# Performance work log

Measured on AMD Instinct MI355X. Metric: run time of the kernel, lower is better.

Reference implementation:

```python
import jax, jax.numpy as jnp
import numpy as np

B0, H0, W0 = 2, 64, 64
C0, E0, N0, R0 = 96, 192, 16, 6


def sass(H, W):
    L = H * W
    o1, o2, o3, o4 = [], [], [], []
    o1i = [-1] * L; o2i = [-1] * L; o3i = [-1] * L; o4i = [-1] * L
    if H % 2 == 1:
        i, j = H - 1, W - 1; jd = 'left'
    else:
        i, j = H - 1, 0; jd = 'right'
    while i > -1:
        idx = i * W + j
        o1i[idx] = len(o1); o1.append(idx)
        if jd == 'right':
            if j < W - 1: j += 1
            else: i -= 1; jd = 'left'
        elif j > 0: j -= 1
        else: i -= 1; jd = 'right'
    i, j = 0, 0; idd = 'down'
    while j < W:
        idx = i * W + j
        o2i[idx] = len(o2); o2.append(idx)
        if idd == 'down':
            if i < H - 1: i += 1
            else: j += 1; idd = 'up'
        elif i > 0: i -= 1
        else: j += 1; idd = 'down'
    for diag in range(H + W - 1):
        for i in range(min(diag + 1, H)):
            j = diag - i
            if j < W:
                idx = i * W + j
                o3i[idx] = len(o3); o3.append(idx)
    for diag in range(H + W - 1):
        for i in range(min(diag + 1, H)):
            j = diag - i
            if j < W:
                idx = i * W + (W - j - 1)
                o4i[idx] = len(o4); o4.append(idx)
    return (o1, o2, o3, o4), (o1i, o2i, o3i, o4i)


def pool_mat(n_in, n_out):
    # adaptive avg pool 1D weighting matrix (torch AdaptiveAvgPool2d semantics)
    P = np.zeros((n_out, n_in), np.float32)
    for i in range(n_out):
        s = (i * n_in) // n_out
        e = -(-((i + 1) * n_in) // n_out)
        P[i, s:e] = 1.0 / (e - s)
    return jnp.asarray(P)


def gconv(x, w, groups, pad):
    return jax.lax.conv_general_dilated(
        x, w, (1, 1), [pad[0], pad[1]],
        dimension_numbers=('NCHW', 'OIHW', 'NCHW'),
        feature_group_count=groups)


def selective_scan(u, delta, A, Bm, Cm, D, delta_bias):
    # u, delta: [B,E,L]; A: [E,N]; Bm, Cm: [B,N,L]; D, delta_bias: [E]
    delta = jax.nn.softplus(delta + delta_bias[None, :, None])
    dA = jnp.exp(jnp.einsum('bel,en->blen', delta, A))          # [B,L,E,N]
    dBu = jnp.einsum('bel,bnl,bel->blen', delta, Bm, u)          # [B,L,E,N]
    def comb(c1, c2):
        a1, b1 = c1; a2, b2 = c2
        return a1 * a2, a2 * b1 + b2
    _, h = jax.lax.associative_scan(comb, (dA, dBu), axis=1)
    return jnp.einsum('blen,bnl->bel', h, Cm) + D[None, :, None] * u


def local_cluster(xc, sim_alpha, sim_beta, f_w, f_b, v_w, v_b, p_w, p_b, w_size=8, K=5):
    Bb, C, H, W = xc.shape
    w, h = H // w_size, W // w_size
    # 'b e (Wg w) (Hg h) -> (b Wg Hg) e w h'
    x = xc.reshape(Bb, C, w_size, w, w_size, h).transpose(0, 2, 4, 1, 3, 5)
    x = x.reshape(Bb * w_size * w_size, C, w, h)
    x1, x2 = jnp.split(x, 2, axis=1)
    f = jnp.einsum('oc,bcwh->bowh', f_w, x1) + f_b[None, :, None, None]
    v = jnp.einsum('oc,bcwh->bowh', v_w, x2) + v_b[None, :, None, None]
    Pw, Ph = pool_mat(w, K), pool_mat(h, K)
    bb, cc = f.shape[0], f.shape[1]
    P = w * h
    cen = jnp.einsum('iw,bcwh,jh->bcij', Pw, f, Ph).reshape(bb, cc, K * K).transpose(0, 2, 1)
    vc = jnp.einsum('iw,bcwh,jh->bcij', Pw, v, Ph).reshape(bb, cc, K * K).transpose(0, 2, 1)
    ff = f.reshape(bb, cc, P).transpose(0, 2, 1)
    nrm = lambda t: t / jnp.maximum(jnp.linalg.norm(t, axis=-1, keepdims=True), 1e-12)
    sim = jax.nn.sigmoid(sim_beta + sim_alpha * jnp.einsum('bkc,bpc->bkp', nrm(cen), nrm(ff)))
    mask = jax.nn.one_hot(jnp.argmax(sim, axis=1), K * K, dtype=sim.dtype).transpose(0, 2, 1)
    sim = sim * mask
    v2 = v.reshape(bb, cc, P).transpose(0, 2, 1)
    agg = (jnp.einsum('bkp,bpc->bkc', sim, v2) + vc) / (sim.sum(-1, keepdims=True) + 1.0)
    out = jnp.einsum('bkc,bkp->bpc', agg, sim)                   # [bb,P,cc]
    out = out.transpose(0, 2, 1).reshape(bb, cc, w, h)
    out = out.reshape(Bb, w_size, w_size, cc, w, h).transpose(0, 3, 1, 4, 2, 5).reshape(Bb, cc, H, W)
    out = jnp.einsum('oc,bchw->bohw', p_w, out) + p_b[None, :, None, None]
    return out.reshape(Bb, C * 0 + p_w.shape[0], H * W)


def _forward(x, conv_h_w, conv_v_w, conv_d1_w, conv_d2_w, fuse_w, in_proj_w, x_proj_w,
             dt_proj_w, dt_proj_b, A_log, D, direction_Bs, out_proj_w,
             sim_alpha, sim_beta, f_w, f_b, v_w, v_b, p_w, p_b,
             cluster_proj_w, cluster_proj_b, branch_channel, ln_w, ln_b, H, W):
    Bt, L, C = x.shape
    E, N = A_log.shape
    R = dt_proj_w.shape[1]
    silu = jax.nn.silu
    x2d = x.reshape(Bt, H, W, C).transpose(0, 3, 1, 2)
    xh = silu(gconv(x2d, conv_h_w, C, ((0, 0), (3, 3))))
    xv = silu(gconv(x2d, conv_v_w, C, ((3, 3), (0, 0))))
    xd1 = silu(gconv(x2d, conv_d1_w, C, ((3, 3), (3, 3))))
    xd2 = silu(gconv(x2d, conv_d2_w, C, ((3, 3), (3, 3))))
    x_conv = jnp.einsum('oc,bchw->bohw', fuse_w, jnp.concatenate([xh, xv, xd1, xd2], 1))
    seq = x_conv.transpose(0, 2, 3, 1).reshape(Bt, L, C)
    xz = seq @ in_proj_w.T
    xp, zp = jnp.split(xz, 2, axis=-1)
    xdbl = xp @ x_proj_w.T
    dt = xdbl[..., :R] @ dt_proj_w.T + dt_proj_b          # bias applied here AND as delta_bias (faithful)
    dt = dt.transpose(0, 2, 1)                            # [B,E,L]
    Bs = xdbl[..., R:R + N].transpose(0, 2, 1)            # [B,N,L]
    Cs = xdbl[..., R + N:].transpose(0, 2, 1)             # [B,N,L]
    A = -jnp.exp(A_log)
    orders, invs = sass(H, W)
    ys = jnp.zeros_like(xp)
    for d in range(4):
        o = jnp.asarray(orders[d], jnp.int32)
        inv = jnp.asarray(invs[d], jnp.int32)
        u = jnp.take(xp, o, axis=1).transpose(0, 2, 1)    # [B,E,L], reordered u only (faithful)
        y = selective_scan(u, dt, A, Bs + direction_Bs[d][None, :, None], Cs, D, dt_proj_b)
        ys = ys + jnp.take(y.transpose(0, 2, 1), inv, axis=1)
    cl = local_cluster(x_conv, sim_alpha, sim_beta, f_w, f_b, v_w, v_b, p_w, p_b)
    cl = cl.transpose(0, 2, 1) @ cluster_proj_w.T + cluster_proj_b
    wch = jax.nn.softmax(branch_channel, axis=0)
    ln = lambda t: (t - t.mean(-1, keepdims=True)) / jnp.sqrt(t.var(-1, keepdims=True) + 1e-5) * ln_w + ln_b
    y = wch[0] * ln(ys) + wch[1] * ln(zp) + wch[2] * ln(cl)
    return y @ out_proj_w.T


def setup_inputs() -> dict:
    key = jax.random.key(0)
    ks = iter(jax.random.split(key, 32))
    def nrm(shape, s=0.02):
        return jax.random.normal(next(ks), shape, jnp.float32) * s
    C, E, N, R = C0, E0, N0, R0
    return {
        'x': jax.random.normal(next(ks), (B0, H0 * W0, C), jnp.float32),
        'H': H0, 'W': W0,
        'conv_h_w': nrm((E, 1, 1, 7), 0.1),
        'conv_v_w': nrm((E, 1, 7, 1), 0.1),
        'conv_d1_w': nrm((E, 1, 7, 7), 0.05),
        'conv_d2_w': nrm((E, 1, 7, 7), 0.05),
        'fuse_w': nrm((C, 4 * E), 0.02),
        'in_proj_w': nrm((2 * E, C), 0.05),
        'x_proj_w': nrm((R + 2 * N, E), 0.05),
        'dt_proj_w': nrm((E, R), 0.1),
        'dt_proj_b': nrm((E,), 1.0) - 4.0,
        'A_log': jnp.log(jnp.tile(jnp.arange(1, N + 1, dtype=jnp.float32)[None, :], (E, 1))),
        'D': jnp.ones((E,), jnp.float32),
        'direction_Bs': nrm((5, N), 0.02),
        'out_proj_w': nrm((C, E), 0.05),
        'sim_alpha': jnp.ones((1,), jnp.float32),
        'sim_beta': jnp.zeros((1,), jnp.float32),
        'f_w': nrm((C // 16, C // 2), 0.1), 'f_b': jnp.zeros((C // 16,), jnp.float32),
        'v_w': nrm((C // 16, C // 2), 0.1), 'v_b': jnp.zeros((C // 16,), jnp.float32),
        'p_w': nrm((C, C // 16), 0.1), 'p_b': jnp.zeros((C,), jnp.float32),
        'cluster_proj_w': nrm((E, C), 0.05), 'cluster_proj_b': jnp.zeros((E,), jnp.float32),
        'branch_channel': jnp.ones((3, E), jnp.float32),
        'ln_w': jnp.ones((E,), jnp.float32), 'ln_b': jnp.zeros((E,), jnp.float32),
    }


def reference(x, H, W, conv_h_w, conv_v_w, conv_d1_w, conv_d2_w, fuse_w, in_proj_w, x_proj_w,
              dt_proj_w, dt_proj_b, A_log, D, direction_Bs, out_proj_w,
              sim_alpha, sim_beta, f_w, f_b, v_w, v_b, p_w, p_b,
              cluster_proj_w, cluster_proj_b, branch_channel, ln_w, ln_b):
    return _forward(x, conv_h_w, conv_v_w, conv_d1_w, conv_d2_w, fuse_w, in_proj_w, x_proj_w,
                    dt_proj_w, dt_proj_b, A_log, D, direction_Bs, out_proj_w,
                    sim_alpha, sim_beta, f_w, f_b, v_w, v_b, p_w, p_b,
                    cluster_proj_w, cluster_proj_b, branch_channel, ln_w, ln_b, H, W)
```

## Files before the change

kernel.cpp:

```cpp
#include <hip/hip_runtime.h>
#include <hip/hip_bf16.h>

#define Bc   2
#define Hc   64
#define Wc   64
#define Lc   4096
#define Cc   96
#define Ec   192
#define Nc   16
#define CATc 768
#define CHUNK 16
#define NCH  256
#define XJ   38

__device__ __forceinline__ int inv_d0(int l) {
    int i = l >> 6, j = l & 63;
    int k = 63 - i;
    int m = (k & 1) ? (63 - j) : j;
    return k * 64 + m;
}
__device__ __forceinline__ int inv_d1(int l) {
    int i = l >> 6, j = l & 63;
    int m = (j & 1) ? (63 - i) : i;
    return j * 64 + m;
}
__device__ __forceinline__ int diag_off(int d) {
    return (d <= 63) ? (d * (d + 1) / 2) : (4096 - (127 - d) * (128 - d) / 2);
}
__device__ __forceinline__ int inv_d2(int l) {
    int i = l >> 6, j = l & 63;
    int d = i + j;
    int st = d > 63 ? d - 63 : 0;
    return diag_off(d) + (i - st);
}
__device__ __forceinline__ int inv_d3(int l) {
    int i = l >> 6, jj = l & 63;
    int j = 63 - jj;
    int d = i + j;
    int st = d > 63 ? d - 63 : 0;
    return diag_off(d) + (i - st);
}

__global__ __launch_bounds__(256) void setup_kernel(
    int* __restrict__ ord, const float* __restrict__ wout,
    float* __restrict__ woutT, const float* __restrict__ fw,
    float* __restrict__ fwT) {
    if (blockIdx.x < 16) {
        int l = blockIdx.x * 256 + threadIdx.x;
        ord[0 * Lc + inv_d0(l)] = l;
        ord[1 * Lc + inv_d1(l)] = l;
        ord[2 * Lc + inv_d2(l)] = l;
        ord[3 * Lc + inv_d3(l)] = l;
    } else if (blockIdx.x < 88) {
        int idx = (blockIdx.x - 16) * 256 + threadIdx.x;
        if (idx < Ec * Cc) {
            int k = idx / Cc, o = idx % Cc;
            woutT[idx] = wout[o * Ec + k];
        }
    } else {
        int idx = (blockIdx.x - 88) * 256 + threadIdx.x;
        int k = idx / Cc, o = idx % Cc;
        fwT[idx] = fw[o * CATc + k];
    }
}

__global__ __launch_bounds__(256) void conv_kernel(
    const float* __restrict__ x, const float* __restrict__ wh,
    const float* __restrict__ wv, const float* __restrict__ wd1,
    const float* __restrict__ wd2, float* __restrict__ cat) {
    int tile = blockIdx.x, ic = blockIdx.y, b = blockIdx.z;
    int th0 = (tile >> 2) * 16, tw0 = (tile & 3) * 16;
    __shared__ float S[22][24];
    int tid = threadIdx.x;
    for (int idx = tid; idx < 22 * 22; idx += 256) {
        int r = idx / 22, c = idx % 22;
        int gh = th0 + r - 3, gw = tw0 + c - 3;
        float v = 0.f;
        if (gh >= 0 && gh < 64 && gw >= 0 && gw < 64)
            v = x[((size_t)b * Lc + gh * 64 + gw) * Cc + ic];
        S[r][c] = v;
    }
    __syncthreads();
    int ti = tid >> 4, tj = tid & 15;
    int pix = (th0 + ti) * 64 + (tw0 + tj);
    for (int s = 0; s < 2; s++) {
        int o = 2 * ic + s;
        float ah = 0.f, av = 0.f, a1 = 0.f, a2 = 0.f;
#pragma unroll
        for (int t = 0; t < 7; t++) {
            ah += S[ti + 3][tj + t] * wh[o * 7 + t];
            av += S[ti + t][tj + 3] * wv[o * 7 + t];
        }
#pragma unroll
        for (int r = 0; r < 7; r++)
#pragma unroll
            for (int c2 = 0; c2 < 7; c2++) {
                float sv = S[ti + r][tj + c2];
                a1 += sv * wd1[o * 49 + r * 7 + c2];
                a2 += sv * wd2[o * 49 + r * 7 + c2];
            }
        cat[((size_t)b * CATc + 0 * Ec + o) * Lc + pix] = ah / (1.f + __expf(-ah));
        cat[((size_t)b * CATc + 1 * Ec + o) * Lc + pix] = av / (1.f + __expf(-av));
        cat[((size_t)b * CATc + 2 * Ec + o) * Lc + pix] = a1 / (1.f + __expf(-a1));
        cat[((size_t)b * CATc + 3 * Ec + o) * Lc + pix] = a2 / (1.f + __expf(-a2));
    }
}

__global__ __launch_bounds__(256) void fuse_part(
    const float* __restrict__ cat, const float* __restrict__ fwT,
    float* __restrict__ pxconv) {
    int l  = blockIdx.x * 256 + threadIdx.x;
    int kc = blockIdx.y;
    int b  = blockIdx.z >> 1;
    int o0 = (blockIdx.z & 1) * 48;
    float acc[48];
#pragma unroll
    for (int j = 0; j < 48; j++) acc[j] = 0.f;
    const float* csrc = cat + ((size_t)b * CATc + kc * 96) * Lc + l;
    const float* wsrc = fwT + (size_t)(kc * 96) * Cc + o0;
#pragma unroll 4
    for (int k = 0; k < 96; k++) {
        float v = csrc[(size_t)k * Lc];
        const float* wr = wsrc + (size_t)k * Cc;
#pragma unroll
        for (int j = 0; j < 48; j++) acc[j] += v * wr[j];
    }
    float* dst = pxconv + (((size_t)kc * Bc + b) * Cc + o0) * Lc + l;
#pragma unroll
    for (int j = 0; j < 48; j++) dst[(size_t)j * Lc] = acc[j];
}

__global__ __launch_bounds__(256) void fuse_reduce(
    const float* __restrict__ pxconv, float* __restrict__ xconv) {
    size_t idx = ((size_t)blockIdx.x * 256 + threadIdx.x) * 4;
    const size_t stride = (size_t)Bc * Cc * Lc;
    float4 s = *(const float4*)(pxconv + idx);
#pragma unroll
    for (int k = 1; k < 8; k++) {
        float4 v = *(const float4*)(pxconv + idx + (size_t)k * stride);
        s.x += v.x; s.y += v.y; s.z += v.z; s.w += v.w;
    }
    *(float4*)(xconv + idx) = s;
}

__global__ __launch_bounds__(256) void inproj_kernel(
    const float* __restrict__ xconv, const float* __restrict__ w,
    float* __restrict__ xp, float* __restrict__ zp) {
    int l = blockIdx.x * 256 + threadIdx.x;
    int o0 = blockIdx.y * 8;
    int b = blockIdx.z;
    float acc[8];
#pragma unroll
    for (int j = 0; j < 8; j++) acc[j] = 0.f;
#pragma unroll 4
    for (int c = 0; c < Cc; c += 2) {
        float v0 = xconv[((size_t)b * Cc + c) * Lc + l];
        float v1 = xconv[((size_t)b * Cc + c + 1) * Lc + l];
#pragma unroll
        for (int j = 0; j < 8; j++) {
            acc[j] += v0 * w[(o0 + j) * Cc + c] + v1 * w[(o0 + j) * Cc + c + 1];
        }
    }
#pragma unroll
    for (int j = 0; j < 8; j++) {
        int o = o0 + j;
        if (o < Ec) xp[((size_t)b * Lc + l) * Ec + o] = acc[j];
        else        zp[((size_t)b * Lc + l) * Ec + (o - Ec)] = acc[j];
    }
}

__global__ __launch_bounds__(256) void xdbl_kernel(
    const float* __restrict__ xp, const float* __restrict__ xw,
    const float* __restrict__ dtw, const float* __restrict__ dtb,
    float* __restrict__ delta, float* __restrict__ Bst, float* __restrict__ Cst) {
    int rb = blockIdx.x;
    __shared__ float S[32][193];
    __shared__ float dt6s[32][6];
    const float* src = xp + (size_t)rb * 32 * Ec;
    for (int idx = threadIdx.x; idx < 32 * Ec / 4; idx += 256) {
        int fl = idx * 4;
        int r = fl / Ec, c = fl % Ec;
        float4 v = *(const float4*)(src + fl);
        S[r][c] = v.x; S[r][c + 1] = v.y; S[r][c + 2] = v.z; S[r][c + 3] = v.w;
    }
    __syncthreads();
    for (int t = threadIdx.x; t < 32 * XJ; t += 256) {
        int r = t / XJ, j = t % XJ;
        const float* wrow = xw + j * Ec;
        float s = 0.f;
#pragma unroll 4
        for (int c = 0; c < Ec; c++) s += S[r][c] * wrow[c];
        int row = rb * 32 + r;
        if (j < 6)       dt6s[r][j] = s;
        else if (j < 22) Bst[row * Nc + (j - 6)] = s;
        else             Cst[row * Nc + (j - 22)] = s;
    }
    __syncthreads();
    for (int idx = threadIdx.x; idx < 32 * Ec; idx += 256) {
        int r = idx / Ec, e = idx % Ec;
        const float* w = dtw + e * 6;
        float s = 2.f * dtb[e];
#pragma unroll
        for (int rr = 0; rr < 6; rr++) s += dt6s[r][rr] * w[rr];
        delta[(size_t)(rb * 32 + r) * Ec + e] = (s > 20.f) ? s : log1pf(__expf(s));
    }
}


__global__ __launch_bounds__(192) void scan_part1(
    const float* __restrict__ xp, const int* __restrict__ ord,
    const float* __restrict__ delta, const float* __restrict__ Bst,
    const float* __restrict__ A_log, const float* __restrict__ dirB,
    float* __restrict__ hend, float* __restrict__ Pend) {
    int chunk = blockIdx.x, b = blockIdx.y, d = blockIdx.z;
    int e = threadIdx.x;
    __shared__ int lord[CHUNK];
    if (threadIdx.x < CHUNK) lord[threadIdx.x] = ord[d * Lc + chunk * CHUNK + threadIdx.x];
    __syncthreads();
    float Aen[Nc], h[Nc], P[Nc], Bd[Nc];
#pragma unroll
    for (int n = 0; n < Nc; n++) {
        Aen[n] = -__expf(A_log[e * Nc + n]);
        Bd[n] = dirB[d * Nc + n];
        h[n] = 0.f; P[n] = 1.f;
    }
    const float* dl  = delta + (size_t)b * Lc * Ec;
    const float* xpb = xp + (size_t)b * Lc * Ec;
    const float* Bb  = Bst + (size_t)b * Lc * Nc;
    int l0 = chunk * CHUNK;
#pragma unroll 2
    for (int t = 0; t < CHUNK; t++) {
        int l = l0 + t;
        float de = dl[(size_t)l * Ec + e];
        float uu = xpb[(size_t)lord[t] * Ec + e];
        float dub = de * uu;
        const float* Brow = Bb + (size_t)l * Nc;
#pragma unroll
        for (int n = 0; n < Nc; n++) {
            float dA = __expf(de * Aen[n]);
            h[n] = dA * h[n] + dub * (Brow[n] + Bd[n]);
            P[n] *= dA;
        }
    }
    size_t base = ((size_t)(d * Bc + b) * NCH + chunk) * 3072 + e;
#pragma unroll
    for (int n = 0; n < Nc; n++) hend[base + n * Ec] = h[n];
    if (d == 0) {
        size_t pb = ((size_t)b * NCH + chunk) * 3072 + e;
#pragma unroll
        for (int n = 0; n < Nc; n++) Pend[pb + n * Ec] = P[n];
    }
}

__global__ __launch_bounds__(256) void scan_mid(
    float* __restrict__ hend, const float* __restrict__ Pend) {
    int blk = blockIdx.x;
    int sub = blk % 12, db = blk / 12;
    int b = db & 1;
    int pair = sub * 256 + threadIdx.x;
    size_t base  = (size_t)db * NCH * 3072 + pair;
    size_t pbase = (size_t)b * NCH * 3072 + pair;
    float h = 0.f;
    for (int c = 0; c < NCH; c++) {
        float hc = hend[base + (size_t)c * 3072];
        float P  = Pend[pbase + (size_t)c * 3072];
        hend[base + (size_t)c * 3072] = h;
        h = P * h + hc;
    }
}

__global__ __launch_bounds__(192) void scan_part2(
    const float* __restrict__ xp, const int* __restrict__ ord,
    const float* __restrict__ delta, const float* __restrict__ Bst,
    const float* __restrict__ Cst, const float* __restrict__ A_log,
    const float* __restrict__ Dp, const float* __restrict__ dirB,
    const float* __restrict__ hend, float* __restrict__ ydir) {
    int chunk = blockIdx.x, b = blockIdx.y, d = blockIdx.z;
    int e = threadIdx.x;
    __shared__ int lord[CHUNK];
    if (threadIdx.x < CHUNK) lord[threadIdx.x] = ord[d * Lc + chunk * CHUNK + threadIdx.x];
    __syncthreads();
    float Aen[Nc], h[Nc], Bd[Nc];
    size_t base = ((size_t)(d * Bc + b) * NCH + chunk) * 3072 + e;
#pragma unroll
    for (int n = 0; n < Nc; n++) {
        Aen[n] = -__expf(A_log[e * Nc + n]);
        Bd[n] = dirB[d * Nc + n];
        h[n] = hend[base + n * Ec];
    }
    float De = Dp[e];
    const float* dl  = delta + (size_t)b * Lc * Ec;
    const float* xpb = xp + (size_t)b * Lc * Ec;
    const float* Bb  = Bst + (size_t)b * Lc * Nc;
    const float* Cb  = Cst + (size_t)b * Lc * Nc;
    float* yo = ydir + ((size_t)(d * Bc + b) * Lc) * Ec + e;
    int l0 = chunk * CHUNK;
#pragma unroll 2
    for (int t = 0; t < CHUNK; t++) {
        int l = l0 + t;
        float de = dl[(size_t)l * Ec + e];
        float uu = xpb[(size_t)lord[t] * Ec + e];
        float dub = de * uu;
        const float* Brow = Bb + (size_t)l * Nc;
        const float* Crow = Cb + (size_t)l * Nc;
        float acc = De * uu;
#pragma unroll
        for (int n = 0; n < Nc; n++) {
            float dA = __expf(de * Aen[n]);
            h[n] = dA * h[n] + dub * (Brow[n] + Bd[n]);
            acc += h[n] * Crow[n];
        }
        yo[(size_t)l * Ec] = acc;
    }
}

__global__ __launch_bounds__(64) void cluster_kernel(
    const float* __restrict__ xconv,
    const float* __restrict__ fwp, const float* __restrict__ fbp,
    const float* __restrict__ vwp, const float* __restrict__ vbp,
    const float* __restrict__ pwp, const float* __restrict__ pbp,
    const float* __restrict__ alphap, const float* __restrict__ betap,
    float* __restrict__ c96) {
    int g = blockIdx.x;
    int b = g >> 6, Wg = (g >> 3) & 7, Hg = g & 7;
    int p = threadIdx.x;
    int wi = p >> 3, hj = p & 7;
    int lsp = (Wg * 8 + wi) * 64 + (Hg * 8 + hj);
    __shared__ float fS[64][6], vS[64][6];
    __shared__ float cen[25][6], vc[25][6], cnorm[25];
    __shared__ float simb[64];
    __shared__ int kb[64];
    __shared__ float agg[25][6];
    float fr[6], vr[6];
#pragma unroll
    for (int oc = 0; oc < 6; oc++) { fr[oc] = fbp[oc]; vr[oc] = vbp[oc]; }
    for (int c = 0; c < 48; c++) {
        float v1 = xconv[((size_t)b * Cc + c) * Lc + lsp];
        float v2 = xconv[((size_t)b * Cc + 48 + c) * Lc + lsp];
#pragma unroll
        for (int oc = 0; oc < 6; oc++) {
            fr[oc] += v1 * fwp[oc * 48 + c];
            vr[oc] += v2 * vwp[oc * 48 + c];
        }
    }
#pragma unroll
    for (int oc = 0; oc < 6; oc++) { fS[p][oc] = fr[oc]; vS[p][oc] = vr[oc]; }
    __syncthreads();
    const int bs[5] = {0, 1, 3, 4, 6}, be[5] = {2, 4, 5, 7, 8};
    for (int t = p; t < 150; t += 64) {
        int k = t / 6, oc = t % 6;
        int ki = k / 5, kj = k % 5;
        float sf = 0.f, sv = 0.f;
        int cnt = 0;
        for (int ii = bs[ki]; ii < be[ki]; ii++)
            for (int jj = bs[kj]; jj < be[kj]; jj++) {
                sf += fS[ii * 8 + jj][oc];
                sv += vS[ii * 8 + jj][oc];
                cnt++;
            }
        cen[k][oc] = sf / cnt;
        vc[k][oc] = sv / cnt;
    }
    __syncthreads();
    if (p < 25) {
        float s = 0.f;
#pragma unroll
        for (int oc = 0; oc < 6; oc++) s += cen[p][oc] * cen[p][oc];
        cnorm[p] = 1.f / fmaxf(sqrtf(s), 1e-12f);
    }
    __syncthreads();
    float fn2 = 0.f;
#pragma unroll
    for (int oc = 0; oc < 6; oc++) fn2 += fr[oc] * fr[oc];
    float finv = 1.f / fmaxf(sqrtf(fn2), 1e-12f);
    float alpha = alphap[0], beta = betap[0];
    float best = -1.f;
    int bestk = 0;
    for (int k = 0; k < 25; k++) {
        float dot = 0.f;
#pragma unroll
        for (int oc = 0; oc < 6; oc++) dot += cen[k][oc] * fr[oc];
        float xv = beta + alpha * dot * cnorm[k] * finv;
        float s = 1.f / (1.f + __expf(-xv));
        if (s > best) { best = s; bestk = k; }
    }
    simb[p] = best;
    kb[p] = bestk;
    __syncthreads();
    if (p < 25) {
        float sum_s = 0.f;
        float av[6];
#pragma unroll
        for (int oc = 0; oc < 6; oc++) av[oc] = vc[p][oc];
        for (int q = 0; q < 64; q++) {
            if (kb[q] == p) {
                float s = simb[q];
                sum_s += s;
#pragma unroll
                for (int oc = 0; oc < 6; oc++) av[oc] += s * vS[q][oc];
            }
        }
        float invd = 1.f / (sum_s + 1.f);
#pragma unroll
        for (int oc = 0; oc < 6; oc++) agg[p][oc] = av[oc] * invd;
    }
    __syncthreads();
    float outp[6];
#pragma unroll
    for (int oc = 0; oc < 6; oc++) outp[oc] = agg[kb[p]][oc] * simb[p];
    float* orow = c96 + ((size_t)b * Lc + lsp) * Cc;
    for (int oo = 0; oo < Cc; oo++) {
        float s = pbp[oo];
#pragma unroll
        for (int oc = 0; oc < 6; oc++) s += outp[oc] * pwp[oo * 6 + oc];
        orow[oo] = s;
    }
}

__global__ __launch_bounds__(256) void clproj_kernel(
    const float* __restrict__ c96, const float* __restrict__ w,
    const float* __restrict__ bias, float* __restrict__ cl) {
    int l = blockIdx.x * 256 + threadIdx.x;
    int o0 = blockIdx.y * 8;
    int b = blockIdx.z;
    const float* row = c96 + ((size_t)b * Lc + l) * Cc;
    float acc[8];
#pragma unroll
    for (int j = 0; j < 8; j++) acc[j] = bias[o0 + j];
#pragma unroll 4
    for (int c = 0; c < Cc; c += 2) {
        float v0 = row[c], v1 = row[c + 1];
#pragma unroll
        for (int j = 0; j < 8; j++) {
            acc[j] += v0 * w[(o0 + j) * Cc + c] + v1 * w[(o0 + j) * Cc + c + 1];
        }
    }
#pragma unroll
    for (int j = 0; j < 8; j++)
        cl[((size_t)b * Lc + l) * Ec + o0 + j] = acc[j];
}

__global__ __launch_bounds__(256) void final_kernel(
    const float* __restrict__ ydir, const float* __restrict__ zp,
    const float* __restrict__ cl, const float* __restrict__ bc,
    const float* __restrict__ lnw, const float* __restrict__ lnb,
    const float* __restrict__ woutT, float* __restrict__ out) {
    __shared__ float comb[4][Ec];
    int wave = threadIdx.x >> 6, lane = threadIdx.x & 63;
    int row = blockIdx.x * 4 + wave;
    int b = row >> 12, lp = row & (Lc - 1);
    int iv0 = inv_d0(lp), iv1 = inv_d1(lp), iv2 = inv_d2(lp), iv3 = inv_d3(lp);
    const float* y0 = ydir + ((size_t)(0 * Bc + b) * Lc + iv0) * Ec;
    const float* y1 = ydir + ((size_t)(1 * Bc + b) * Lc + iv1) * Ec;
    const float* y2 = ydir + ((size_t)(2 * Bc + b) * Lc + iv2) * Ec;
    const float* y3 = ydir + ((size_t)(3 * Bc + b) * Lc + iv3) * Ec;
    const float* zr = zp + ((size_t)b * Lc + lp) * Ec;
    const float* cr = cl + ((size_t)b * Lc + lp) * Ec;
    float ys[3], zv[3], cv[3];
    float s1 = 0, s2 = 0, z1 = 0, z2 = 0, c1 = 0, c2 = 0;
#pragma unroll
    for (int t = 0; t < 3; t++) {
        int i = lane + t * 64;
        float v = y0[i] + y1[i] + y2[i] + y3[i];
        ys[t] = v; s1 += v; s2 += v * v;
        float z = zr[i]; zv[t] = z; z1 += z; z2 += z * z;
        float c = cr[i]; cv[t] = c; c1 += c; c2 += c * c;
    }
#pragma unroll
    for (int o = 32; o >= 1; o >>= 1) {
        s1 += __shfl_xor(s1, o, 64); s2 += __shfl_xor(s2, o, 64);
        z1 += __shfl_xor(z1, o, 64); z2 += __shfl_xor(z2, o, 64);
        c1 += __shfl_xor(c1, o, 64); c2 += __shfl_xor(c2, o, 64);
    }
    const float invE = 1.f / (float)Ec;
    float ym = s1 * invE, yvr = rsqrtf(s2 * invE - ym * ym + 1e-5f);
    float zm = z1 * invE, zvr = rsqrtf(z2 * invE - zm * zm + 1e-5f);
    float cm = c1 * invE, cvr = rsqrtf(c2 * invE - cm * cm + 1e-5f);
#pragma unroll
    for (int t = 0; t < 3; t++) {
        int i = lane + t * 64;
        float g = lnw[i], bb = lnb[i];
        float a0 = (ys[t] - ym) * yvr * g + bb;
        float a1 = (zv[t] - zm) * zvr * g + bb;
        float a2 = (cv[t] - cm) * cvr * g + bb;
        float w0 = bc[i], w1 = bc[Ec + i], w2 = bc[2 * Ec + i];
        float mx = fmaxf(w0, fmaxf(w1, w2));
        float e0 = __expf(w0 - mx), e1 = __expf(w1 - mx), e2 = __expf(w2 - mx);
        float inv = 1.f / (e0 + e1 + e2);
        comb[wave][i] = (e0 * a0 + e1 * a1 + e2 * a2) * inv;
    }
    __syncthreads();
    float r0 = 0.f, r1 = 0.f;
#pragma unroll 4
    for (int k = 0; k < Ec; k++) {
        float cvk = comb[wave][k];
        float w0 = woutT[k * Cc + lane];
        float w1 = woutT[k * Cc + 64 + lane];
        r0 += cvk * w0;
        r1 += cvk * w1;
    }
    float* orow = out + (size_t)row * Cc;
    orow[lane] = r0;
    if (lane < 32) orow[64 + lane] = r1;
}

extern "C" void kernel_launch(void* const* d_in, const int* in_sizes, int n_in,
                              void* d_out, int out_size, void* d_ws, size_t ws_size,
                              hipStream_t stream) {
    const float* x       = (const float*)d_in[0];
    const float* wh      = (const float*)d_in[3];
    const float* wv      = (const float*)d_in[4];
    const float* wd1     = (const float*)d_in[5];
    const float* wd2     = (const float*)d_in[6];
    const float* fw      = (const float*)d_in[7];
    const float* ipw     = (const float*)d_in[8];
    const float* xw      = (const float*)d_in[9];
    const float* dtw     = (const float*)d_in[10];
    const float* dtb     = (const float*)d_in[11];
    const float* A_log   = (const float*)d_in[12];
    const float* Dp      = (const float*)d_in[13];
    const float* dirB    = (const float*)d_in[14];
    const float* wout    = (const float*)d_in[15];
    const float* alphap  = (const float*)d_in[16];
    const float* betap   = (const float*)d_in[17];
    const float* fwp     = (const float*)d_in[18];
    const float* fbp     = (const float*)d_in[19];
    const float* vwp     = (const float*)d_in[20];
    const float* vbp     = (const float*)d_in[21];
    const float* pwp     = (const float*)d_in[22];
    const float* pbp     = (const float*)d_in[23];
    const float* clw     = (const float*)d_in[24];
    const float* clb     = (const float*)d_in[25];
    const float* bc      = (const float*)d_in[26];
    const float* lnw     = (const float*)d_in[27];
    const float* lnb     = (const float*)d_in[28];
    float* out = (float*)d_out;

    float* wsf = (float*)d_ws;
    size_t off = 0;
    int* ord      = (int*)wsf;             off += 4 * Lc;
    float* cat    = wsf + off;             off += (size_t)Bc * CATc * Lc;
    float* xconv  = wsf + off;             off += (size_t)Bc * Cc * Lc;
    float* xp     = wsf + off;             off += (size_t)Bc * Lc * Ec;
    float* zpb    = wsf + off;             off += (size_t)Bc * Lc * Ec;
    float* deltab = wsf + off;             off += (size_t)Bc * Lc * Ec;
    float* Bst    = wsf + off;             off += (size_t)Bc * Lc * Nc;
    float* Cst    = wsf + off;             off += (size_t)Bc * Lc * Nc;
    float* hend   = wsf + off;             off += (size_t)4 * Bc * NCH * Ec * Nc;
    float* Pend   = wsf + off;             off += (size_t)Bc * NCH * Ec * Nc;
    float* woutT  = wsf + off;             off += (size_t)Ec * Cc + 64;
    float* fwT    = wsf + off;             off += (size_t)CATc * Cc;
    float* ydir = cat;
    float* c96  = xp;
    float* cl   = deltab;
    float* pxconv = xp;

    setup_kernel<<<376, 256, 0, stream>>>(ord, wout, woutT, fw, fwT);
    conv_kernel<<<dim3(16, 96, 2), 256, 0, stream>>>(x, wh, wv, wd1, wd2, cat);
    fuse_part<<<dim3(16, 8, 4), 256, 0, stream>>>(cat, fwT, pxconv);
    fuse_reduce<<<768, 256, 0, stream>>>(pxconv, xconv);
    inproj_kernel<<<dim3(16, 48, 2), 256, 0, stream>>>(xconv, ipw, xp, zpb);
    xdbl_kernel<<<256, 256, 0, stream>>>(xp, xw, dtw, dtb, deltab, Bst, Cst);
    scan_part1<<<dim3(NCH, 2, 4), 192, 0, stream>>>(xp, ord, deltab, Bst,
                                                    A_log, dirB, hend, Pend);
    scan_mid<<<96, 256, 0, stream>>>(hend, Pend);
    scan_part2<<<dim3(NCH, 2, 4), 192, 0, stream>>>(xp, ord, deltab, Bst, Cst,
                                                    A_log, Dp, dirB, hend, ydir);
    cluster_kernel<<<128, 64, 0, stream>>>(xconv, fwp, fbp, vwp, vbp, pwp, pbp,
                                           alphap, betap, c96);
    clproj_kernel<<<dim3(16, 24, 2), 256, 0, stream>>>(c96, clw, clb, cl);
    final_kernel<<<2048, 256, 0, stream>>>(ydir, zpb, cl, bc, lnw, lnb, woutT, out);
}
```

Before: 407.3 us.

## Merge four scan directions per block and split x_proj into split-K GEMM

The scan kernels now handle all four scan directions in one block, sharing the delta, exp(dA) and B/C loads across four hidden-state sets instead of launching one block per direction. B and C are stored transposed (N-major), and the x_proj projection is restructured into a split-K GEMM over a transposed copy of xp, followed by separate reduce and delta kernels. This cuts repeated exp work and redundant loads, at the cost of four times more register state per thread (possible lower occupancy or spills), fewer scan blocks, and extra kernel launches and intermediate traffic.

```diff
diff --git a/kernel.cpp b/kernel.cpp
--- a/kernel.cpp
+++ b/kernel.cpp
@@ -44,7 +44,8 @@
 __global__ __launch_bounds__(256) void setup_kernel(
     int* __restrict__ ord, const float* __restrict__ wout,
     float* __restrict__ woutT, const float* __restrict__ fw,
-    float* __restrict__ fwT) {
+    float* __restrict__ fwT, const float* __restrict__ xw,
+    float* __restrict__ xwT) {
     if (blockIdx.x < 16) {
         int l = blockIdx.x * 256 + threadIdx.x;
         ord[0 * Lc + inv_d0(l)] = l;
@@ -57,10 +58,16 @@
             int k = idx / Cc, o = idx % Cc;
             woutT[idx] = wout[o * Ec + k];
         }
-    } else {
+    } else if (blockIdx.x < 376) {
         int idx = (blockIdx.x - 88) * 256 + threadIdx.x;
         int k = idx / Cc, o = idx % Cc;
         fwT[idx] = fw[o * CATc + k];
+    } else {
+        int idx = (blockIdx.x - 376) * 256 + threadIdx.x;
+        if (idx < Ec * XJ) {
+            int c = idx / XJ, j = idx % XJ;
+            xwT[idx] = xw[j * Ec + c];
+        }
     }
 }
 
@@ -145,7 +152,7 @@
 
 __global__ __launch_bounds__(256) void inproj_kernel(
     const float* __restrict__ xconv, const float* __restrict__ w,
-    float* __restrict__ xp, float* __restrict__ zp) {
+    float* __restrict__ xp, float* __restrict__ zp, float* __restrict__ xpT) {
     int l = blockIdx.x * 256 + threadIdx.x;
     int o0 = blockIdx.y * 8;
     int b = blockIdx.z;
@@ -164,91 +171,115 @@
 #pragma unroll
     for (int j = 0; j < 8; j++) {
         int o = o0 + j;
-        if (o < Ec) xp[((size_t)b * Lc + l) * Ec + o] = acc[j];
-        else        zp[((size_t)b * Lc + l) * Ec + (o - Ec)] = acc[j];
-    }
-}
-
-__global__ __launch_bounds__(256) void xdbl_kernel(
-    const float* __restrict__ xp, const float* __restrict__ xw,
-    const float* __restrict__ dtw, const float* __restrict__ dtb,
-    float* __restrict__ delta, float* __restrict__ Bst, float* __restrict__ Cst) {
-    int rb = blockIdx.x;
-    __shared__ float S[32][193];
-    __shared__ float dt6s[32][6];
-    const float* src = xp + (size_t)rb * 32 * Ec;
-    for (int idx = threadIdx.x; idx < 32 * Ec / 4; idx += 256) {
-        int fl = idx * 4;
-        int r = fl / Ec, c = fl % Ec;
-        float4 v = *(const float4*)(src + fl);
-        S[r][c] = v.x; S[r][c + 1] = v.y; S[r][c + 2] = v.z; S[r][c + 3] = v.w;
-    }
-    __syncthreads();
-    for (int t = threadIdx.x; t < 32 * XJ; t += 256) {
-        int r = t / XJ, j = t % XJ;
-        const float* wrow = xw + j * Ec;
-        float s = 0.f;
+        if (o < Ec) {
+            xp[((size_t)b * Lc + l) * Ec + o] = acc[j];
+            xpT[(size_t)o * (Bc * Lc) + b * Lc + l] = acc[j];
+        } else {
+            zp[((size_t)b * Lc + l) * Ec + (o - Ec)] = acc[j];
+        }
+    }
+}
+
+__global__ __launch_bounds__(256) void xdbl_gemm(
+    const float* __restrict__ xpT, const float* __restrict__ xwT,
+    float* __restrict__ pxd) {
+    int r  = blockIdx.x * 256 + threadIdx.x;
+    int kc = blockIdx.y;
+    float acc[XJ];
+#pragma unroll
+    for (int j = 0; j < XJ; j++) acc[j] = 0.f;
+    const float* src = xpT + (size_t)(kc * 24) * (Bc * Lc) + r;
+    const float* w   = xwT + kc * 24 * XJ;
 #pragma unroll 4
-        for (int c = 0; c < Ec; c++) s += S[r][c] * wrow[c];
-        int row = rb * 32 + r;
-        if (j < 6)       dt6s[r][j] = s;
-        else if (j < 22) Bst[row * Nc + (j - 6)] = s;
-        else             Cst[row * Nc + (j - 22)] = s;
-    }
-    __syncthreads();
-    for (int idx = threadIdx.x; idx < 32 * Ec; idx += 256) {
-        int r = idx / Ec, e = idx % Ec;
-        const float* w = dtw + e * 6;
-        float s = 2.f * dtb[e];
-#pragma unroll
-        for (int rr = 0; rr < 6; rr++) s += dt6s[r][rr] * w[rr];
-        delta[(size_t)(rb * 32 + r) * Ec + e] = (s > 20.f) ? s : log1pf(__expf(s));
-    }
+    for (int k = 0; k < 24; k++) {
+        float v = src[(size_t)k * (Bc * Lc)];
+        const float* wr = w + k * XJ;
+#pragma unroll
+        for (int j = 0; j < XJ; j++) acc[j] += v * wr[j];
+    }
+    float* dst = pxd + (size_t)kc * XJ * (Bc * Lc) + r;
+#pragma unroll
+    for (int j = 0; j < XJ; j++) dst[(size_t)j * (Bc * Lc)] = acc[j];
+}
+
+__global__ __launch_bounds__(256) void xdbl_reduce(
+    const float* __restrict__ pxd, float* __restrict__ dt6R,
+    float* __restrict__ BstT, float* __restrict__ CstT) {
+    int idx = blockIdx.x * 256 + threadIdx.x;
+    float s = 0.f;
+#pragma unroll
+    for (int kc = 0; kc < 8; kc++) s += pxd[(size_t)kc * XJ * (Bc * Lc) + idx];
+    int j = idx >> 13, r = idx & (Bc * Lc - 1);
+    int b = r >> 12, l = r & (Lc - 1);
+    if (j < 6)       dt6R[j * (Bc * Lc) + r] = s;
+    else if (j < 22) BstT[((size_t)b * Nc + (j - 6)) * Lc + l] = s;
+    else             CstT[((size_t)b * Nc + (j - 22)) * Lc + l] = s;
+}
+
+__global__ __launch_bounds__(192) void delta_kernel(
+    const float* __restrict__ dt6R, const float* __restrict__ dtw,
+    const float* __restrict__ dtb, float* __restrict__ delta) {
+    int r = blockIdx.x;
+    int e = threadIdx.x;
+    const float* w = dtw + e * 6;
+    float s = 2.f * dtb[e];
+#pragma unroll
+    for (int rr = 0; rr < 6; rr++) s += dt6R[rr * (Bc * Lc) + r] * w[rr];
+    delta[(size_t)r * Ec + e] = (s > 20.f) ? s : log1pf(__expf(s));
 }
 
 
 __global__ __launch_bounds__(192) void scan_part1(
     const float* __restrict__ xp, const int* __restrict__ ord,
-    const float* __restrict__ delta, const float* __restrict__ Bst,
+    const float* __restrict__ delta, const float* __restrict__ BstT,
     const float* __restrict__ A_log, const float* __restrict__ dirB,
     float* __restrict__ hend, float* __restrict__ Pend) {
-    int chunk = blockIdx.x, b = blockIdx.y, d = blockIdx.z;
+    int chunk = blockIdx.x, b = blockIdx.y;
     int e = threadIdx.x;
-    __shared__ int lord[CHUNK];
-    if (threadIdx.x < CHUNK) lord[threadIdx.x] = ord[d * Lc + chunk * CHUNK + threadIdx.x];
-    __syncthreads();
-    float Aen[Nc], h[Nc], P[Nc], Bd[Nc];
+    __shared__ int lord[4][CHUNK];
+    if (threadIdx.x < 64) {
+        int d = threadIdx.x >> 4, t = threadIdx.x & 15;
+        lord[d][t] = ord[d * Lc + chunk * CHUNK + t];
+    }
+    __syncthreads();
+    float Aen[Nc], P[Nc];
+    float h0[Nc], h1[Nc], h2[Nc], h3[Nc];
 #pragma unroll
     for (int n = 0; n < Nc; n++) {
         Aen[n] = -__expf(A_log[e * Nc + n]);
-        Bd[n] = dirB[d * Nc + n];
-        h[n] = 0.f; P[n] = 1.f;
+        P[n] = 1.f; h0[n] = 0.f; h1[n] = 0.f; h2[n] = 0.f; h3[n] = 0.f;
     }
     const float* dl  = delta + (size_t)b * Lc * Ec;
     const float* xpb = xp + (size_t)b * Lc * Ec;
-    const float* Bb  = Bst + (size_t)b * Lc * Nc;
+    const float* Bb  = BstT + (size_t)b * Nc * Lc;
     int l0 = chunk * CHUNK;
-#pragma unroll 2
     for (int t = 0; t < CHUNK; t++) {
         int l = l0 + t;
         float de = dl[(size_t)l * Ec + e];
-        float uu = xpb[(size_t)lord[t] * Ec + e];
-        float dub = de * uu;
-        const float* Brow = Bb + (size_t)l * Nc;
+        float du0 = de * xpb[(size_t)lord[0][t] * Ec + e];
+        float du1 = de * xpb[(size_t)lord[1][t] * Ec + e];
+        float du2 = de * xpb[(size_t)lord[2][t] * Ec + e];
+        float du3 = de * xpb[(size_t)lord[3][t] * Ec + e];
 #pragma unroll
         for (int n = 0; n < Nc; n++) {
             float dA = __expf(de * Aen[n]);
-            h[n] = dA * h[n] + dub * (Brow[n] + Bd[n]);
+            float Bn = Bb[(size_t)n * Lc + l];
             P[n] *= dA;
-        }
-    }
-    size_t base = ((size_t)(d * Bc + b) * NCH + chunk) * 3072 + e;
-#pragma unroll
-    for (int n = 0; n < Nc; n++) hend[base + n * Ec] = h[n];
-    if (d == 0) {
-        size_t pb = ((size_t)b * NCH + chunk) * 3072 + e;
-#pragma unroll
-        for (int n = 0; n < Nc; n++) Pend[pb + n * Ec] = P[n];
+            h0[n] = dA * h0[n] + du0 * (Bn + dirB[0 * Nc + n]);
+            h1[n] = dA * h1[n] + du1 * (Bn + dirB[1 * Nc + n]);
+            h2[n] = dA * h2[n] + du2 * (Bn + dirB[2 * Nc + n]);
+            h3[n] = dA * h3[n] + du3 * (Bn + dirB[3 * Nc + n]);
+        }
+    }
+    size_t cb = ((size_t)b * NCH + chunk) * 3072 + e;
+    const size_t dstr = (size_t)Bc * NCH * 3072;
+#pragma unroll
+    for (int n = 0; n < Nc; n++) {
+        hend[cb + 0 * dstr + n * Ec] = h0[n];
+        hend[cb + 1 * dstr + n * Ec] = h1[n];
+        hend[cb + 2 * dstr + n * Ec] = h2[n];
+        hend[cb + 3 * dstr + n * Ec] = h3[n];
+        Pend[cb + n * Ec] = P[n];
     }
 }
 
@@ -271,46 +302,65 @@
 
 __global__ __launch_bounds__(192) void scan_part2(
     const float* __restrict__ xp, const int* __restrict__ ord,
-    const float* __restrict__ delta, const float* __restrict__ Bst,
-    const float* __restrict__ Cst, const float* __restrict__ A_log,
+    const float* __restrict__ delta, const float* __restrict__ BstT,
+    const float* __restrict__ CstT, const float* __restrict__ A_log,
     const float* __restrict__ Dp, const float* __restrict__ dirB,
     const float* __restrict__ hend, float* __restrict__ ydir) {
-    int chunk = blockIdx.x, b = blockIdx.y, d = blockIdx.z;
+    int chunk = blockIdx.x, b = blockIdx.y;
     int e = threadIdx.x;
-    __shared__ int lord[CHUNK];
-    if (threadIdx.x < CHUNK) lord[threadIdx.x] = ord[d * Lc + chunk * CHUNK + threadIdx.x];
-    __syncthreads();
-    float Aen[Nc], h[Nc], Bd[Nc];
-    size_t base = ((size_t)(d * Bc + b) * NCH + chunk) * 3072 + e;
+    __shared__ int lord[4][CHUNK];
+    if (threadIdx.x < 64) {
+        int d = threadIdx.x >> 4, t = threadIdx.x & 15;
+        lord[d][t] = ord[d * Lc + chunk * CHUNK + t];
+    }
+    __syncthreads();
+    float Aen[Nc];
+    float h0[Nc], h1[Nc], h2[Nc], h3[Nc];
+    size_t cb = ((size_t)b * NCH + chunk) * 3072 + e;
+    const size_t dstr = (size_t)Bc * NCH * 3072;
 #pragma unroll
     for (int n = 0; n < Nc; n++) {
         Aen[n] = -__expf(A_log[e * Nc + n]);
-        Bd[n] = dirB[d * Nc + n];
-        h[n] = hend[base + n * Ec];
+        h0[n] = hend[cb + 0 * dstr + n * Ec];
+        h1[n] = hend[cb + 1 * dstr + n * Ec];
+        h2[n] = hend[cb + 2 * dstr + n * Ec];
+        h3[n] = hend[cb + 3 * dstr + n * Ec];
     }
     float De = Dp[e];
     const float* dl  = delta + (size_t)b * Lc * Ec;
     const float* xpb = xp + (size_t)b * Lc * Ec;
-    const float* Bb  = Bst + (size_t)b * Lc * Nc;
-    const float* Cb  = Cst + (size_t)b * Lc * Nc;
-    float* yo = ydir + ((size_t)(d * Bc + b) * Lc) * Ec + e;
+    const float* Bb  = BstT + (size_t)b * Nc * Lc;
+    const float* Cb  = CstT + (size_t)b * Nc * Lc;
+    float* yo0 = ydir + ((size_t)(0 * Bc + b) * Lc) * Ec + e;
+    float* yo1 = ydir + ((size_t)(1 * Bc + b) * Lc) * Ec + e;
+    float* yo2 = ydir + ((size_t)(2 * Bc + b) * Lc) * Ec + e;
+    float* yo3 = ydir + ((size_t)(3 * Bc + b) * Lc) * Ec + e;
     int l0 = chunk * CHUNK;
-#pragma unroll 2
     for (int t = 0; t < CHUNK; t++) {
         int l = l0 + t;
         float de = dl[(size_t)l * Ec + e];
-        float uu = xpb[(size_t)lord[t] * Ec + e];
-        float dub = de * uu;
-        const float* Brow = Bb + (size_t)l * Nc;
-        const float* Crow = Cb + (size_t)l * Nc;
-        float acc = De * uu;
+        float u0 = xpb[(size_t)lord[0][t] * Ec + e];
+        float u1 = xpb[(size_t)lord[1][t] * Ec + e];
+        float u2 = xpb[(size_t)lord[2][t] * Ec + e];
+        float u3 = xpb[(size_t)lord[3][t] * Ec + e];
+        float du0 = de * u0, du1 = de * u1, du2 = de * u2, du3 = de * u3;
+        float a0 = De * u0, a1 = De * u1, a2 = De * u2, a3 = De * u3;
 #pragma unroll
         for (int n = 0; n < Nc; n++) {
             float dA = __expf(de * Aen[n]);
-            h[n] = dA * h[n] + dub * (Brow[n] + Bd[n]);
-            acc += h[n] * Crow[n];
-        }
-        yo[(size_t)l * Ec] = acc;
+            float Bn = Bb[(size_t)n * Lc + l];
+            float Cn = Cb[(size_t)n * Lc + l];
+            h0[n] = dA * h0[n] + du0 * (Bn + dirB[0 * Nc + n]);
+            h1[n] = dA * h1[n] + du1 * (Bn + dirB[1 * Nc + n]);
+            h2[n] = dA * h2[n] + du2 * (Bn + dirB[2 * Nc + n]);
+            h3[n] = dA * h3[n] + du3 * (Bn + dirB[3 * Nc + n]);
+            a0 += h0[n] * Cn; a1 += h1[n] * Cn;
+            a2 += h2[n] * Cn; a3 += h3[n] * Cn;
+        }
+        yo0[(size_t)l * Ec] = a0;
+        yo1[(size_t)l * Ec] = a1;
+        yo2[(size_t)l * Ec] = a2;
+        yo3[(size_t)l * Ec] = a3;
     }
 }
 
@@ -544,28 +594,34 @@
     float* xp     = wsf + off;             off += (size_t)Bc * Lc * Ec;
     float* zpb    = wsf + off;             off += (size_t)Bc * Lc * Ec;
     float* deltab = wsf + off;             off += (size_t)Bc * Lc * Ec;
-    float* Bst    = wsf + off;             off += (size_t)Bc * Lc * Nc;
-    float* Cst    = wsf + off;             off += (size_t)Bc * Lc * Nc;
+    float* BstT   = wsf + off;             off += (size_t)Bc * Lc * Nc;
+    float* CstT   = wsf + off;             off += (size_t)Bc * Lc * Nc;
     float* hend   = wsf + off;             off += (size_t)4 * Bc * NCH * Ec * Nc;
     float* Pend   = wsf + off;             off += (size_t)Bc * NCH * Ec * Nc;
     float* woutT  = wsf + off;             off += (size_t)Ec * Cc + 64;
     float* fwT    = wsf + off;             off += (size_t)CATc * Cc;
+    float* xwT    = wsf + off;             off += (size_t)Ec * XJ + 64;
     float* ydir = cat;
     float* c96  = xp;
     float* cl   = deltab;
     float* pxconv = xp;
-
-    setup_kernel<<<376, 256, 0, stream>>>(ord, wout, woutT, fw, fwT);
+    float* xpT  = hend;
+    float* pxd  = hend + (size_t)Ec * Bc * Lc;
+    float* dt6R = pxd + (size_t)8 * XJ * Bc * Lc;
+
+    setup_kernel<<<405, 256, 0, stream>>>(ord, wout, woutT, fw, fwT, xw, xwT);
     conv_kernel<<<dim3(16, 96, 2), 256, 0, stream>>>(x, wh, wv, wd1, wd2, cat);
     fuse_part<<<dim3(16, 8, 4), 256, 0, stream>>>(cat, fwT, pxconv);
     fuse_reduce<<<768, 256, 0, stream>>>(pxconv, xconv);
-    inproj_kernel<<<dim3(16, 48, 2), 256, 0, stream>>>(xconv, ipw, xp, zpb);
-    xdbl_kernel<<<256, 256, 0, stream>>>(xp, xw, dtw, dtb, deltab, Bst, Cst);
-    scan_part1<<<dim3(NCH, 2, 4), 192, 0, stream>>>(xp, ord, deltab, Bst,
-                                                    A_log, dirB, hend, Pend);
+    inproj_kernel<<<dim3(16, 48, 2), 256, 0, stream>>>(xconv, ipw, xp, zpb, xpT);
+    xdbl_gemm<<<dim3(32, 8), 256, 0, stream>>>(xpT, xwT, pxd);
+    xdbl_reduce<<<1216, 256, 0, stream>>>(pxd, dt6R, BstT, CstT);
+    delta_kernel<<<8192, 192, 0, stream>>>(dt6R, dtw, dtb, deltab);
+    scan_part1<<<dim3(NCH, 2), 192, 0, stream>>>(xp, ord, deltab, BstT,
+                                                 A_log, dirB, hend, Pend);
     scan_mid<<<96, 256, 0, stream>>>(hend, Pend);
-    scan_part2<<<dim3(NCH, 2, 4), 192, 0, stream>>>(xp, ord, deltab, Bst, Cst,
-                                                    A_log, Dp, dirB, hend, ydir);
+    scan_part2<<<dim3(NCH, 2), 192, 0, stream>>>(xp, ord, deltab, BstT, CstT,
+                                                 A_log, Dp, dirB, hend, ydir);
     cluster_kernel<<<128, 64, 0, stream>>>(xconv, fwp, fbp, vwp, vbp, pwp, pbp,
                                            alphap, betap, c96);
     clproj_kernel<<<dim3(16, 24, 2), 256, 0, stream>>>(c96, clw, clb, cl);
```

Result: no change. 402.1 us (-1.3%).
